# Kernel tuning notes

Measured on AMD Instinct MI355X. Metric: run time of the kernel, lower is better.

The kernel has to match this reference:

```python
import jax, jax.numpy as jnp
import numpy as np

E, H, V, KV, B, L = 512, 1024, 50257, 1000, 64, 512


def setup_inputs() -> dict:
    key = jax.random.key(0)
    ks = jax.random.split(key, 32)

    def p(i, shape, scale=0.02):
        return jax.random.normal(ks[i], shape, jnp.float32) * scale

    return {
        # forward args
        "input_ids": jax.random.randint(ks[0], (B,), 0, V),
        "h": p(1, (B, H), 1.0),
        "c": p(2, (B, H), 1.0),
        "k": p(3, (KV, E), 1.0),
        "context_vector": p(4, (B, H), 1.0),
        "encoder_outputs": p(5, (B, L, H), 1.0),
        # parameters (stored [in, out])
        "embedding": p(6, (V, E)),
        "W_ih": p(7, (E, 4 * H)),
        "W_hh": p(8, (H, 4 * H)),
        "b_ih": jnp.zeros((4 * H,), jnp.float32),
        "b_hh": jnp.zeros((4 * H,), jnp.float32),
        # attn MLP: Linear(2H,E) Tanh Linear(E,E) Tanh Linear(E,1)
        "aW1": p(9, (2 * H, E)), "ab1": jnp.zeros((E,), jnp.float32),
        "aW2": p(10, (E, E)), "ab2": jnp.zeros((E,), jnp.float32),
        "aW3": p(11, (E, 1)), "ab3": jnp.zeros((1,), jnp.float32),
        # attn_key MLP: Linear(E+2H,E) Tanh Linear(E,E) Tanh Linear(E,1)
        "kW1": p(12, (E + 2 * H, E)), "kb1": jnp.zeros((E,), jnp.float32),
        "kW2": p(13, (E, E)), "kb2": jnp.zeros((E,), jnp.float32),
        "kW3": p(14, (E, 1)), "kb3": jnp.zeros((1,), jnp.float32),
        # attn_linear: Linear(2H, V)
        "alW": p(15, (2 * H, V)), "alb": jnp.zeros((V,), jnp.float32),
    }


def reference(input_ids, h, c, k, context_vector, encoder_outputs,
              embedding, W_ih, W_hh, b_ih, b_hh,
              aW1, ab1, aW2, ab2, aW3, ab3,
              kW1, kb1, kW2, kb2, kW3, kb3,
              alW, alb):
    b = h.shape[0]
    kv = k.shape[0]
    v = alb.shape[0]

    # embedding lookup (dropout is identity in eval)
    x = embedding[input_ids]                                    # [B,E]

    # LSTMCell (PyTorch gate order: i, f, g, o)
    gates = x @ W_ih + h @ W_hh + b_ih + b_hh                   # [B,4H]
    i_g, f_g, g_g, o_g = jnp.split(gates, 4, axis=1)
    c_t = jax.nn.sigmoid(f_g) * c + jax.nn.sigmoid(i_g) * jnp.tanh(g_g)
    h_t = jax.nn.sigmoid(o_g) * jnp.tanh(c_t)                   # [B,H]

    # additive attention over encoder outputs
    h_ext = jnp.broadcast_to(h_t[:, None, :], encoder_outputs.shape)
    u = jnp.concatenate([encoder_outputs, h_ext], axis=2)       # [B,L,2H]
    u = jnp.tanh(u @ aW1 + ab1)
    u = jnp.tanh(u @ aW2 + ab2)
    u = (u @ aW3 + ab3)[..., 0]                                  # [B,L]
    a_t = jax.nn.softmax(u, axis=1)
    h_ctx = jnp.einsum('bl,blh->bh', a_t, encoder_outputs)       # [B,H]

    # key attention: cat(context, h_t, k) -> MLP -> [B,KV]
    ctx_ext = jnp.broadcast_to(context_vector[:, None, :], (b, kv, context_vector.shape[1]))
    ht_ext = jnp.broadcast_to(h_t[:, None, :], (b, kv, h_t.shape[1]))
    k_ext = jnp.broadcast_to(k[None, :, :], (b, kv, k.shape[1]))
    uk = jnp.concatenate([ctx_ext, ht_ext, k_ext], axis=2)       # [B,KV,E+2H]
    uk = jnp.tanh(uk @ kW1 + kb1)
    uk = jnp.tanh(uk @ kW2 + kb2)
    uk = (uk @ kW3 + kb3)[..., 0]                                # [B,KV]

    # zero-pad key logits into the full vocab (first V-KV entries are zero)
    v_k_t = jnp.concatenate([jnp.zeros((b, v - kv), h_t.dtype), uk], axis=1)

    # key_flag == 'True' path
    o_t = jnp.concatenate([h_t, h_ctx], axis=1) @ alW + alb + v_k_t  # [B,V]
    y_t = jax.nn.log_softmax(o_t, axis=1)
    return (y_t, h_t, c_t)
```

## Files before the change

### kernel.cpp

```cpp
#include <hip/hip_runtime.h>
#include <hip/hip_bf16.h>
#include <math.h>

#define EE 512
#define HH 1024
#define VV 50257
#define KVN 1000
#define BB 64
#define LL 512
#define FH 4096
#define TWOH 2048

typedef __hip_bfloat16 bf16;
typedef short bf16x8 __attribute__((ext_vector_type(8)));
typedef float f32x4  __attribute__((ext_vector_type(4)));

__device__ __forceinline__ float sigm(float x){ return 1.0f/(1.0f+__expf(-x)); }

__device__ __forceinline__ unsigned short f2bf(float f){
  unsigned int u = __float_as_uint(f);
  unsigned int r = (u + 0x7FFFu + ((u >> 16) & 1u)) >> 16;
  return (unsigned short)r;
}

__global__ __launch_bounds__(256)
void k_embed_gates(const int* __restrict__ ids, const float* __restrict__ h,
                   const float* __restrict__ emb,
                   const float* __restrict__ W_ih, const float* __restrict__ W_hh,
                   const float* __restrict__ b_ih, const float* __restrict__ b_hh,
                   float* __restrict__ gates){
  __shared__ float xh[8][1536];
  const int j  = blockIdx.x*256 + threadIdx.x;
  const int b0 = blockIdx.y*8;
  for (int t = threadIdx.x; t < 8*1536; t += 256){
    int bb = t / 1536, kk = t - bb*1536;
    int b = b0 + bb;
    float v;
    if (kk < EE) v = emb[(size_t)ids[b]*EE + kk];
    else         v = h[(size_t)b*HH + (kk-EE)];
    xh[bb][kk] = v;
  }
  __syncthreads();
  float acc[8];
  #pragma unroll
  for (int i=0;i<8;i++) acc[i]=0.f;
  for (int k=0;k<1536;k++){
    float w = (k<EE) ? W_ih[(size_t)k*FH + j] : W_hh[(size_t)(k-EE)*FH + j];
    #pragma unroll
    for (int i=0;i<8;i++) acc[i] += xh[i][k]*w;
  }
  const float bias = b_ih[j] + b_hh[j];
  #pragma unroll
  for (int i=0;i<8;i++) gates[(size_t)(b0+i)*FH + j] = acc[i] + bias;
}

__global__ __launch_bounds__(256)
void k_lstm(const float* __restrict__ gates, const float* __restrict__ c_in,
            float* __restrict__ hout, float* __restrict__ cout){
  int idx = blockIdx.x*256 + threadIdx.x;
  int b = idx >> 10, hh = idx & 1023;
  const float* g = gates + (size_t)b*FH;
  float ig = g[hh], fg = g[HH+hh], gg = g[2*HH+hh], og = g[3*HH+hh];
  float ct = sigm(fg)*c_in[idx] + sigm(ig)*tanhf(gg);
  float ht = sigm(og)*tanhf(ct);
  hout[idx] = ht;
  cout[idx] = ct;
}

__global__ __launch_bounds__(256)
void k_q1p1(const float* __restrict__ ht, const float* __restrict__ ctx,
            const float* __restrict__ aW1, const float* __restrict__ ab1,
            const float* __restrict__ kW1, const float* __restrict__ kb1,
            float* __restrict__ q1, float* __restrict__ p1){
  int e = blockIdx.x*256 + threadIdx.x;
  int b = blockIdx.y;
  float aq = 0.f, ap = 0.f;
  for (int k2 = 0; k2 < HH; ++k2){
    float hv = ht[(size_t)b*HH + k2];
    float cv = ctx[(size_t)b*HH + k2];
    aq += hv * aW1[(size_t)(HH+k2)*EE + e];
    ap += cv * kW1[(size_t)k2*EE + e];
    ap += hv * kW1[(size_t)(HH+k2)*EE + e];
  }
  q1[(size_t)b*EE + e] = aq + ab1[e];
  p1[(size_t)b*EE + e] = ap + kb1[e];
}

__global__ __launch_bounds__(256)
void k_p2(const float* __restrict__ kin, const float* __restrict__ kW1,
          float* __restrict__ p2){
  int e  = blockIdx.x*256 + threadIdx.x;
  int kv = blockIdx.y;
  float a = 0.f;
  for (int k2 = 0; k2 < EE; ++k2)
    a += kin[(size_t)kv*EE + k2] * kW1[(size_t)(TWOH+k2)*EE + e];
  p2[(size_t)kv*EE + e] = a;
}

__global__ __launch_bounds__(256)
void k_uk1(const float* __restrict__ p1, const float* __restrict__ p2,
           bf16* __restrict__ uk1){
  int idx = blockIdx.x*256 + threadIdx.x;
  int e   = idx & (EE-1);
  int r   = idx >> 9;
  int b   = r / KVN;
  int kv  = r - b*KVN;
  float v = tanhf(p1[(size_t)b*EE + e] + p2[(size_t)kv*EE + e]);
  uk1[idx] = __float2bfloat16(v);
}

__global__ __launch_bounds__(256)
void k_transpose_bf16(const float* __restrict__ W, bf16* __restrict__ Wt,
                      int K, int N){
  __shared__ float t[32][33];
  int k0 = blockIdx.y*32, n0 = blockIdx.x*32;
  int tx = threadIdx.x & 31, ty = threadIdx.x >> 5;
  #pragma unroll
  for (int i=0;i<4;i++){
    int kk = ty + i*8;
    t[kk][tx] = W[(size_t)(k0+kk)*N + n0 + tx];
  }
  __syncthreads();
  #pragma unroll
  for (int i=0;i<4;i++){
    int nn = ty + i*8;
    Wt[(size_t)(n0+nn)*K + k0 + tx] = __float2bfloat16(t[tx][nn]);
  }
}

__global__ __launch_bounds__(256)
void k_mfma_tanh_dot(const bf16* __restrict__ A, const bf16* __restrict__ Wt,
                     const float* __restrict__ bias, const float* __restrict__ w3,
                     float* __restrict__ logits){
  __shared__ short As[128*40];
  __shared__ short Bs[128*40];
  __shared__ float red[128*33];
  const int tid  = threadIdx.x;
  const int lane = tid & 63, wid = tid >> 6;
  const int wm = wid >> 1, wn = wid & 1;
  const int quad = lane >> 4, l16 = lane & 15;
  const int m0 = blockIdx.y*128, n0 = blockIdx.x*128;

  f32x4 acc[4][4] = {};
  for (int k0 = 0; k0 < 512; k0 += 32){
    #pragma unroll
    for (int it = 0; it < 2; ++it){
      int task = tid + it*256;
      int row = task >> 2, cg = task & 3;
      *(bf16x8*)(As + row*40 + cg*8) =
        *(const bf16x8*)((const short*)A + (size_t)(m0+row)*512 + k0 + cg*8);
      *(bf16x8*)(Bs + row*40 + cg*8) =
        *(const bf16x8*)((const short*)Wt + (size_t)(n0+row)*512 + k0 + cg*8);
    }
    __syncthreads();
    bf16x8 af[4], bfr[4];
    #pragma unroll
    for (int mt=0; mt<4; ++mt)
      af[mt] = *(const bf16x8*)(As + (wm*64 + mt*16 + l16)*40 + quad*8);
    #pragma unroll
    for (int nt=0; nt<4; ++nt)
      bfr[nt] = *(const bf16x8*)(Bs + (wn*64 + nt*16 + l16)*40 + quad*8);
    #pragma unroll
    for (int mt=0; mt<4; ++mt)
      #pragma unroll
      for (int nt=0; nt<4; ++nt)
        acc[mt][nt] = __builtin_amdgcn_mfma_f32_16x16x32_bf16(af[mt], bfr[nt], acc[mt][nt], 0, 0, 0);
    __syncthreads();
  }
  float bv[4], wv[4];
  #pragma unroll
  for (int nt=0; nt<4; ++nt){
    int n = n0 + wn*64 + nt*16 + l16;
    bv[nt] = bias[n]; wv[nt] = w3[n];
  }
  #pragma unroll
  for (int mt=0; mt<4; ++mt){
    #pragma unroll
    for (int r=0; r<4; ++r){
      float s = 0.f;
      #pragma unroll
      for (int nt=0; nt<4; ++nt)
        s += tanhf(acc[mt][nt][r] + bv[nt]) * wv[nt];
      int rowL = wm*64 + mt*16 + quad*4 + r;
      red[rowL*33 + wn*16 + l16] = s;
    }
  }
  __syncthreads();
  if (tid < 128){
    float s = 0.f;
    #pragma unroll
    for (int j=0;j<32;j++) s += red[tid*33 + j];
    atomicAdd(&logits[m0 + tid], s);
  }
}

__global__ __launch_bounds__(256)
void k_mfma_a1(const float* __restrict__ enc, const bf16* __restrict__ Wt,
               const float* __restrict__ q1, bf16* __restrict__ U1){
  __shared__ short As[128*40];
  __shared__ short Bs[128*40];
  const int tid  = threadIdx.x;
  const int lane = tid & 63, wid = tid >> 6;
  const int wm = wid >> 1, wn = wid & 1;
  const int quad = lane >> 4, l16 = lane & 15;
  const int m0 = blockIdx.y*128, n0 = blockIdx.x*128;

  f32x4 acc[4][4] = {};
  for (int k0 = 0; k0 < 1024; k0 += 32){
    #pragma unroll
    for (int it = 0; it < 4; ++it){
      int task = tid + it*256;
      int row = task >> 3, g = task & 7;
      float4 f = *(const float4*)(enc + (size_t)(m0+row)*1024 + k0 + g*4);
      uint2 pk;
      pk.x = (unsigned int)f2bf(f.x) | ((unsigned int)f2bf(f.y) << 16);
      pk.y = (unsigned int)f2bf(f.z) | ((unsigned int)f2bf(f.w) << 16);
      *(uint2*)(As + row*40 + g*4) = pk;
    }
    #pragma unroll
    for (int it = 0; it < 2; ++it){
      int task = tid + it*256;
      int row = task >> 2, cg = task & 3;
      *(bf16x8*)(Bs + row*40 + cg*8) =
        *(const bf16x8*)((const short*)Wt + (size_t)(n0+row)*1024 + k0 + cg*8);
    }
    __syncthreads();
    bf16x8 af[4], bfr[4];
    #pragma unroll
    for (int mt=0; mt<4; ++mt)
      af[mt] = *(const bf16x8*)(As + (wm*64 + mt*16 + l16)*40 + quad*8);
    #pragma unroll
    for (int nt=0; nt<4; ++nt)
      bfr[nt] = *(const bf16x8*)(Bs + (wn*64 + nt*16 + l16)*40 + quad*8);
    #pragma unroll
    for (int mt=0; mt<4; ++mt)
      #pragma unroll
      for (int nt=0; nt<4; ++nt)
        acc[mt][nt] = __builtin_amdgcn_mfma_f32_16x16x32_bf16(af[mt], bfr[nt], acc[mt][nt], 0, 0, 0);
    __syncthreads();
  }
  const int b = m0 >> 9;
  const float* q1r = q1 + (size_t)b*EE;
  #pragma unroll
  for (int mt=0; mt<4; ++mt){
    #pragma unroll
    for (int r=0; r<4; ++r){
      int m = m0 + wm*64 + mt*16 + quad*4 + r;
      #pragma unroll
      for (int nt=0; nt<4; ++nt){
        int n = n0 + wn*64 + nt*16 + l16;
        U1[(size_t)m*EE + n] = __float2bfloat16(tanhf(acc[mt][nt][r] + q1r[n]));
      }
    }
  }
}

__global__ __launch_bounds__(256)
void k_init_logits(float* __restrict__ ulog, float* __restrict__ uklog,
                   const float* __restrict__ ab3, const float* __restrict__ kb3){
  int i = blockIdx.x*256 + threadIdx.x;
  if (i < BB*LL)  ulog[i]  = ab3[0];
  if (i < BB*KVN) uklog[i] = kb3[0];
}

__global__ __launch_bounds__(256)
void k_softmax(float* __restrict__ ulog){
  __shared__ float sdata[256];
  int b = blockIdx.x, tid = threadIdx.x;
  float* row = ulog + (size_t)b*LL;
  float v0 = row[tid], v1 = row[tid+256];
  sdata[tid] = fmaxf(v0, v1);
  __syncthreads();
  for (int s=128;s>0;s>>=1){ if (tid<s) sdata[tid]=fmaxf(sdata[tid],sdata[tid+s]); __syncthreads(); }
  float mx = sdata[0];
  __syncthreads();
  float e0 = __expf(v0-mx), e1 = __expf(v1-mx);
  sdata[tid] = e0+e1;
  __syncthreads();
  for (int s=128;s>0;s>>=1){ if (tid<s) sdata[tid]+=sdata[tid+s]; __syncthreads(); }
  float inv = 1.f/sdata[0];
  row[tid]     = e0*inv;
  row[tid+256] = e1*inv;
}

__global__ __launch_bounds__(256)
void k_hctx(const float* __restrict__ a, const float* __restrict__ enc,
            float* __restrict__ hctx){
  int hh = blockIdx.x*256 + threadIdx.x;
  int b  = blockIdx.y;
  float s = 0.f;
  for (int l=0;l<LL;l++)
    s += a[(size_t)b*LL + l] * enc[((size_t)b*LL + l)*HH + hh];
  hctx[(size_t)b*HH + hh] = s;
}

__global__ __launch_bounds__(256)
void k_hcatT(const float* __restrict__ ht, const float* __restrict__ hctx,
             float* __restrict__ hcatT){
  int idx = blockIdx.x*256 + threadIdx.x;
  int b = idx & 63, kk = idx >> 6;
  float v = (kk < HH) ? ht[(size_t)b*HH + kk] : hctx[(size_t)b*HH + (kk-HH)];
  hcatT[idx] = v;
}

__global__ __launch_bounds__(256)
void k_final(const float* __restrict__ hcatT, const float* __restrict__ alW,
             const float* __restrict__ alb, const float* __restrict__ uklog,
             float* __restrict__ y){
  __shared__ float Hs[16][64];
  __shared__ float Ws[16][64];
  const int tid = threadIdx.x;
  const int tx = tid & 15, ty = tid >> 4;
  const int n0 = blockIdx.x * 64;
  float acc[4][4] = {};
  for (int k0 = 0; k0 < TWOH; k0 += 16){
    #pragma unroll
    for (int i=0;i<4;i++){
      int t = tid + i*256;
      int kk = t >> 6, cc = t & 63;
      Hs[kk][cc] = hcatT[(size_t)(k0+kk)*64 + cc];
      int v = n0 + cc;
      Ws[kk][cc] = (v < VV) ? alW[(size_t)(k0+kk)*VV + v] : 0.f;
    }
    __syncthreads();
    #pragma unroll
    for (int kk=0;kk<16;kk++){
      float4 hb = *(const float4*)(&Hs[kk][ty*4]);
      float4 wv = *(const float4*)(&Ws[kk][tx*4]);
      float ha[4] = {hb.x, hb.y, hb.z, hb.w};
      float wa[4] = {wv.x, wv.y, wv.z, wv.w};
      #pragma unroll
      for (int i=0;i<4;i++)
        #pragma unroll
        for (int j=0;j<4;j++)
          acc[i][j] += ha[i]*wa[j];
    }
    __syncthreads();
  }
  #pragma unroll
  for (int j=0;j<4;j++){
    int v = n0 + tx*4 + j;
    if (v < VV){
      float bias = alb[v];
      int dk = v - (VV - KVN);
      #pragma unroll
      for (int i=0;i<4;i++){
        int b = ty*4 + i;
        float o = acc[i][j] + bias;
        if (dk >= 0) o += uklog[b*KVN + dk];
        y[(size_t)b*VV + v] = o;
      }
    }
  }
}

__global__ __launch_bounds__(256)
void k_logsoftmax(float* __restrict__ y){
  __shared__ float sdata[256];
  int b = blockIdx.x, tid = threadIdx.x;
  float* row = y + (size_t)b*VV;
  float m = -1e30f;
  for (int i=tid;i<VV;i+=256) m = fmaxf(m, row[i]);
  sdata[tid] = m; __syncthreads();
  for (int s=128;s>0;s>>=1){ if (tid<s) sdata[tid]=fmaxf(sdata[tid],sdata[tid+s]); __syncthreads(); }
  float mx = sdata[0]; __syncthreads();
  float sum = 0.f;
  for (int i=tid;i<VV;i+=256) sum += __expf(row[i]-mx);
  sdata[tid] = sum; __syncthreads();
  for (int s=128;s>0;s>>=1){ if (tid<s) sdata[tid]+=sdata[tid+s]; __syncthreads(); }
  float lse = mx + logf(sdata[0]);
  for (int i=tid;i<VV;i+=256) row[i] -= lse;
}

extern "C" void kernel_launch(void* const* d_in, const int* in_sizes, int n_in,
                              void* d_out, int out_size, void* d_ws, size_t ws_size,
                              hipStream_t stream) {
  const int*   ids  = (const int*)  d_in[0];
  const float* h    = (const float*)d_in[1];
  const float* c    = (const float*)d_in[2];
  const float* kin  = (const float*)d_in[3];
  const float* ctx  = (const float*)d_in[4];
  const float* enc  = (const float*)d_in[5];
  const float* emb  = (const float*)d_in[6];
  const float* W_ih = (const float*)d_in[7];
  const float* W_hh = (const float*)d_in[8];
  const float* b_ih = (const float*)d_in[9];
  const float* b_hh = (const float*)d_in[10];
  const float* aW1  = (const float*)d_in[11];
  const float* ab1  = (const float*)d_in[12];
  const float* aW2  = (const float*)d_in[13];
  const float* ab2  = (const float*)d_in[14];
  const float* aW3  = (const float*)d_in[15];
  const float* ab3  = (const float*)d_in[16];
  const float* kW1  = (const float*)d_in[17];
  const float* kb1  = (const float*)d_in[18];
  const float* kW2  = (const float*)d_in[19];
  const float* kb2  = (const float*)d_in[20];
  const float* kW3  = (const float*)d_in[21];
  const float* kb3  = (const float*)d_in[22];
  const float* alW  = (const float*)d_in[23];
  const float* alb  = (const float*)d_in[24];

  float* y      = (float*)d_out;
  float* ht_out = y + (size_t)BB*VV;
  float* ct_out = ht_out + (size_t)BB*HH;

  char* w = (char*)d_ws;
  float* gates = (float*)w;  w += (size_t)BB*FH*4;
  float* q1    = (float*)w;  w += (size_t)BB*EE*4;
  float* p1    = (float*)w;  w += (size_t)BB*EE*4;
  float* p2    = (float*)w;  w += (size_t)KVN*EE*4;
  float* ulog  = (float*)w;  w += (size_t)BB*LL*4;
  float* uklog = (float*)w;  w += (size_t)BB*KVN*4;
  float* hctx  = (float*)w;  w += (size_t)BB*HH*4;
  float* hcatT = (float*)w;  w += (size_t)TWOH*BB*4;
  bf16*  U1    = (bf16*)w;   w += (size_t)BB*LL*EE*2;
  bf16*  UK1   = (bf16*)w;   w += (size_t)BB*KVN*EE*2;
  bf16*  aW1t  = (bf16*)w;   w += (size_t)EE*HH*2;
  bf16*  aW2t  = (bf16*)w;   w += (size_t)EE*EE*2;
  bf16*  kW2t  = (bf16*)w;   w += (size_t)EE*EE*2;

  k_transpose_bf16<<<dim3(EE/32, HH/32), 256, 0, stream>>>(aW1, aW1t, HH, EE);
  k_transpose_bf16<<<dim3(EE/32, EE/32), 256, 0, stream>>>(aW2, aW2t, EE, EE);
  k_transpose_bf16<<<dim3(EE/32, EE/32), 256, 0, stream>>>(kW2, kW2t, EE, EE);

  k_embed_gates<<<dim3(FH/256, BB/8), 256, 0, stream>>>(ids, h, emb, W_ih, W_hh, b_ih, b_hh, gates);
  k_lstm<<<(BB*HH)/256, 256, 0, stream>>>(gates, c, ht_out, ct_out);

  k_init_logits<<<(BB*KVN)/256 + 1, 256, 0, stream>>>(ulog, uklog, ab3, kb3);

  k_q1p1<<<dim3(EE/256, BB), 256, 0, stream>>>(ht_out, ctx, aW1, ab1, kW1, kb1, q1, p1);
  k_p2<<<dim3(EE/256, KVN), 256, 0, stream>>>(kin, kW1, p2);

  k_uk1<<<(BB*KVN*EE)/256, 256, 0, stream>>>(p1, p2, UK1);
  k_mfma_tanh_dot<<<dim3(4, (BB*KVN)/128), 256, 0, stream>>>(UK1, kW2t, kb2, kW3, uklog);

  k_mfma_a1<<<dim3(4, (BB*LL)/128), 256, 0, stream>>>(enc, aW1t, q1, U1);
  k_mfma_tanh_dot<<<dim3(4, (BB*LL)/128), 256, 0, stream>>>(U1, aW2t, ab2, aW3, ulog);
  k_softmax<<<BB, 256, 0, stream>>>(ulog);
  k_hctx<<<dim3(HH/256, BB), 256, 0, stream>>>(ulog, enc, hctx);

  k_hcatT<<<(TWOH*BB)/256, 256, 0, stream>>>(ht_out, hctx, hcatT);
  k_final<<<(VV + 63)/64, 256, 0, stream>>>(hcatT, alW, alb, uklog, y);
  k_logsoftmax<<<BB, 256, 0, stream>>>(y);
}
```

Baseline: 1.731 ms.

## Use MFMA for vocab projection, fuse key tanh, split-K gates, parallel log-softmax

Several independent changes at once. The final vocab projection now runs on bf16 MFMA with split-K and atomic accumulation into a bias-initialized output. The key-attention tanh is fused into the MFMA A-tile load, which removes the large UK1 intermediate. The LSTM gate GEMM is restructured into split-K tiles with atomics, and log-softmax is split into multi-block partial, combine and apply passes. The trade-offs are extra atomic traffic on the 64x50257 output, reduced precision on the vocab projection, and a tanh recomputed for every N-tile block.

```diff
diff --git a/kernel.cpp b/kernel.cpp
--- a/kernel.cpp
+++ b/kernel.cpp
@@ -24,34 +24,67 @@
 }
 
 __global__ __launch_bounds__(256)
+void k_gates_init(const float* __restrict__ b_ih, const float* __restrict__ b_hh,
+                  float* __restrict__ gates){
+  int i = blockIdx.x*256 + threadIdx.x;
+  int j = i & (FH-1);
+  gates[i] = b_ih[j] + b_hh[j];
+}
+
+__global__ __launch_bounds__(256)
 void k_embed_gates(const int* __restrict__ ids, const float* __restrict__ h,
                    const float* __restrict__ emb,
                    const float* __restrict__ W_ih, const float* __restrict__ W_hh,
-                   const float* __restrict__ b_ih, const float* __restrict__ b_hh,
                    float* __restrict__ gates){
-  __shared__ float xh[8][1536];
-  const int j  = blockIdx.x*256 + threadIdx.x;
-  const int b0 = blockIdx.y*8;
-  for (int t = threadIdx.x; t < 8*1536; t += 256){
-    int bb = t / 1536, kk = t - bb*1536;
-    int b = b0 + bb;
-    float v;
-    if (kk < EE) v = emb[(size_t)ids[b]*EE + kk];
-    else         v = h[(size_t)b*HH + (kk-EE)];
-    xh[bb][kk] = v;
+  __shared__ float Xs[64][68];
+  __shared__ float Ws[64][68];
+  const int tid = threadIdx.x;
+  const int nbase = blockIdx.x*64;
+  const int kbase = blockIdx.y*64;
+  {
+    int b = tid >> 2;
+    int kof = (tid & 3)*16;
+    int id = ids[b];
+    #pragma unroll
+    for (int i=0;i<16;i++){
+      int kg = kbase + kof + i;
+      float v = (kg < EE) ? emb[(size_t)id*EE + kg] : h[(size_t)b*HH + (kg-EE)];
+      Xs[kof+i][b] = v;
+    }
+  }
+  {
+    int n = tid & 63;
+    int kr0 = tid >> 6;
+    #pragma unroll
+    for (int i=0;i<16;i++){
+      int kr = kr0 + i*4;
+      int kg = kbase + kr;
+      float v = (kg < EE) ? W_ih[(size_t)kg*FH + nbase + n]
+                          : W_hh[(size_t)(kg-EE)*FH + nbase + n];
+      Ws[kr][n] = v;
+    }
   }
   __syncthreads();
-  float acc[8];
-  #pragma unroll
-  for (int i=0;i<8;i++) acc[i]=0.f;
-  for (int k=0;k<1536;k++){
-    float w = (k<EE) ? W_ih[(size_t)k*FH + j] : W_hh[(size_t)(k-EE)*FH + j];
-    #pragma unroll
-    for (int i=0;i<8;i++) acc[i] += xh[i][k]*w;
-  }
-  const float bias = b_ih[j] + b_hh[j];
-  #pragma unroll
-  for (int i=0;i<8;i++) gates[(size_t)(b0+i)*FH + j] = acc[i] + bias;
+  const int tx = tid & 15, ty = tid >> 4;
+  float acc[4][4] = {};
+  for (int k=0;k<64;k++){
+    float4 a4 = *(const float4*)(&Xs[k][ty*4]);
+    float4 w4 = *(const float4*)(&Ws[k][tx*4]);
+    float aa[4] = {a4.x,a4.y,a4.z,a4.w};
+    float ww[4] = {w4.x,w4.y,w4.z,w4.w};
+    #pragma unroll
+    for (int i=0;i<4;i++)
+      #pragma unroll
+      for (int j=0;j<4;j++)
+        acc[i][j] += aa[i]*ww[j];
+  }
+  #pragma unroll
+  for (int i=0;i<4;i++){
+    int b = ty*4 + i;
+    #pragma unroll
+    for (int j=0;j<4;j++)
+      atomicAdd(&gates[(size_t)b*FH + nbase + tx*4 + j], acc[i][j]);
+  }
 }
 
 __global__ __launch_bounds__(256)
@@ -98,18 +131,6 @@
 }
 
 __global__ __launch_bounds__(256)
-void k_uk1(const float* __restrict__ p1, const float* __restrict__ p2,
-           bf16* __restrict__ uk1){
-  int idx = blockIdx.x*256 + threadIdx.x;
-  int e   = idx & (EE-1);
-  int r   = idx >> 9;
-  int b   = r / KVN;
-  int kv  = r - b*KVN;
-  float v = tanhf(p1[(size_t)b*EE + e] + p2[(size_t)kv*EE + e]);
-  uk1[idx] = __float2bfloat16(v);
-}
-
-__global__ __launch_bounds__(256)
 void k_transpose_bf16(const float* __restrict__ W, bf16* __restrict__ Wt,
                       int K, int N){
   __shared__ float t[32][33];
@@ -134,7 +155,6 @@
                      float* __restrict__ logits){
   __shared__ short As[128*40];
   __shared__ short Bs[128*40];
-  __shared__ float red[128*33];
   const int tid  = threadIdx.x;
   const int lane = tid & 63, wid = tid >> 6;
   const int wm = wid >> 1, wn = wid & 1;
@@ -181,16 +201,88 @@
       #pragma unroll
       for (int nt=0; nt<4; ++nt)
         s += tanhf(acc[mt][nt][r] + bv[nt]) * wv[nt];
-      int rowL = wm*64 + mt*16 + quad*4 + r;
-      red[rowL*33 + wn*16 + l16] = s;
-    }
-  }
-  __syncthreads();
-  if (tid < 128){
-    float s = 0.f;
-    #pragma unroll
-    for (int j=0;j<32;j++) s += red[tid*33 + j];
-    atomicAdd(&logits[m0 + tid], s);
+      #pragma unroll
+      for (int off=8; off>=1; off>>=1) s += __shfl_xor(s, off, 16);
+      if (l16 == 0){
+        int row = wm*64 + mt*16 + quad*4 + r;
+        atomicAdd(&logits[m0 + row], s);
+      }
+    }
+  }
+}
+
+__global__ __launch_bounds__(256)
+void k_mfma_key(const float* __restrict__ p1, const float* __restrict__ p2,
+                const bf16* __restrict__ Wt,
+                const float* __restrict__ bias, const float* __restrict__ w3,
+                float* __restrict__ logits){
+  __shared__ short As[128*40];
+  __shared__ short Bs[128*40];
+  const int tid  = threadIdx.x;
+  const int lane = tid & 63, wid = tid >> 6;
+  const int wm = wid >> 1, wn = wid & 1;
+  const int quad = lane >> 4, l16 = lane & 15;
+  const int m0 = blockIdx.y*128, n0 = blockIdx.x*128;
+
+  f32x4 acc[4][4] = {};
+  for (int k0 = 0; k0 < 512; k0 += 32){
+    #pragma unroll
+    for (int it = 0; it < 2; ++it){
+      int grp = tid + it*256;
+      int row = grp >> 2, cg = grp & 3;
+      int r = m0 + row;
+      int b = r / KVN;
+      int kv = r - b*KVN;
+      int e = k0 + cg*8;
+      float4 a0 = *(const float4*)(p1 + (size_t)b*EE + e);
+      float4 a1 = *(const float4*)(p1 + (size_t)b*EE + e + 4);
+      float4 c0 = *(const float4*)(p2 + (size_t)kv*EE + e);
+      float4 c1 = *(const float4*)(p2 + (size_t)kv*EE + e + 4);
+      bf16x8 v;
+      v[0]=(short)f2bf(tanhf(a0.x+c0.x)); v[1]=(short)f2bf(tanhf(a0.y+c0.y));
+      v[2]=(short)f2bf(tanhf(a0.z+c0.z)); v[3]=(short)f2bf(tanhf(a0.w+c0.w));
+      v[4]=(short)f2bf(tanhf(a1.x+c1.x)); v[5]=(short)f2bf(tanhf(a1.y+c1.y));
+      v[6]=(short)f2bf(tanhf(a1.z+c1.z)); v[7]=(short)f2bf(tanhf(a1.w+c1.w));
+      *(bf16x8*)(As + row*40 + cg*8) = v;
+      *(bf16x8*)(Bs + row*40 + cg*8) =
+        *(const bf16x8*)((const short*)Wt + (size_t)(n0+row)*512 + k0 + cg*8);
+    }
+    __syncthreads();
+    bf16x8 af[4], bfr[4];
+    #pragma unroll
+    for (int mt=0; mt<4; ++mt)
+      af[mt] = *(const bf16x8*)(As + (wm*64 + mt*16 + l16)*40 + quad*8);
+    #pragma unroll
+    for (int nt=0; nt<4; ++nt)
+      bfr[nt] = *(const bf16x8*)(Bs + (wn*64 + nt*16 + l16)*40 + quad*8);
+    #pragma unroll
+    for (int mt=0; mt<4; ++mt)
+      #pragma unroll
+      for (int nt=0; nt<4; ++nt)
+        acc[mt][nt] = __builtin_amdgcn_mfma_f32_16x16x32_bf16(af[mt], bfr[nt], acc[mt][nt], 0, 0, 0);
+    __syncthreads();
+  }
+  float bv[4], wv[4];
+  #pragma unroll
+  for (int nt=0; nt<4; ++nt){
+    int n = n0 + wn*64 + nt*16 + l16;
+    bv[nt] = bias[n]; wv[nt] = w3[n];
+  }
+  #pragma unroll
+  for (int mt=0; mt<4; ++mt){
+    #pragma unroll
+    for (int r=0; r<4; ++r){
+      float s = 0.f;
+      #pragma unroll
+      for (int nt=0; nt<4; ++nt)
+        s += tanhf(acc[mt][nt][r] + bv[nt]) * wv[nt];
+      #pragma unroll
+      for (int off=8; off>=1; off>>=1) s += __shfl_xor(s, off, 16);
+      if (l16 == 0){
+        int row = wm*64 + mt*16 + quad*4 + r;
+        atomicAdd(&logits[m0 + row], s);
+      }
+    }
   }
 }
 
@@ -295,81 +387,138 @@
 }
 
 __global__ __launch_bounds__(256)
-void k_hcatT(const float* __restrict__ ht, const float* __restrict__ hctx,
-             float* __restrict__ hcatT){
+void k_hcat_bf16(const float* __restrict__ ht, const float* __restrict__ hctx,
+                 bf16* __restrict__ hcatb){
   int idx = blockIdx.x*256 + threadIdx.x;
-  int b = idx & 63, kk = idx >> 6;
+  int b = idx >> 11, kk = idx & 2047;
   float v = (kk < HH) ? ht[(size_t)b*HH + kk] : hctx[(size_t)b*HH + (kk-HH)];
-  hcatT[idx] = v;
-}
-
-__global__ __launch_bounds__(256)
-void k_final(const float* __restrict__ hcatT, const float* __restrict__ alW,
-             const float* __restrict__ alb, const float* __restrict__ uklog,
-             float* __restrict__ y){
-  __shared__ float Hs[16][64];
-  __shared__ float Ws[16][64];
-  const int tid = threadIdx.x;
-  const int tx = tid & 15, ty = tid >> 4;
-  const int n0 = blockIdx.x * 64;
-  float acc[4][4] = {};
-  for (int k0 = 0; k0 < TWOH; k0 += 16){
-    #pragma unroll
-    for (int i=0;i<4;i++){
-      int t = tid + i*256;
-      int kk = t >> 6, cc = t & 63;
-      Hs[kk][cc] = hcatT[(size_t)(k0+kk)*64 + cc];
-      int v = n0 + cc;
-      Ws[kk][cc] = (v < VV) ? alW[(size_t)(k0+kk)*VV + v] : 0.f;
-    }
-    __syncthreads();
-    #pragma unroll
-    for (int kk=0;kk<16;kk++){
-      float4 hb = *(const float4*)(&Hs[kk][ty*4]);
-      float4 wv = *(const float4*)(&Ws[kk][tx*4]);
-      float ha[4] = {hb.x, hb.y, hb.z, hb.w};
-      float wa[4] = {wv.x, wv.y, wv.z, wv.w};
-      #pragma unroll
-      for (int i=0;i<4;i++)
+  hcatb[idx] = __float2bfloat16(v);
+}
+
+__global__ __launch_bounds__(256)
+void k_y_init(const float* __restrict__ alb, const float* __restrict__ uklog,
+              float* __restrict__ y){
+  int idx = blockIdx.x*256 + threadIdx.x;
+  if (idx >= BB*VV) return;
+  int b = idx / VV;
+  int v = idx - b*VV;
+  float o = alb[v];
+  int dk = v - (VV - KVN);
+  if (dk >= 0) o += uklog[b*KVN + dk];
+  y[idx] = o;
+}
+
+__global__ __launch_bounds__(256)
+void k_final_mfma(const bf16* __restrict__ hcatb, const float* __restrict__ alW,
+                  float* __restrict__ y){
+  __shared__ short As[64*40];
+  __shared__ float Bs[32*133];
+  const int tid  = threadIdx.x;
+  const int lane = tid & 63, wid = tid >> 6;
+  const int quad = lane >> 4, l16 = lane & 15;
+  const int n0 = blockIdx.x*128;
+  const int kc0 = blockIdx.y*512;
+
+  f32x4 acc[4][2] = {};
+  for (int k0 = 0; k0 < 512; k0 += 32){
+    {
+      int row = tid >> 2, cg = tid & 3;
+      *(bf16x8*)(As + row*40 + cg*8) =
+        *(const bf16x8*)((const short*)hcatb + (size_t)row*TWOH + kc0 + k0 + cg*8);
+    }
+    #pragma unroll
+    for (int i=0;i<16;i++){
+      int flat = tid + i*256;
+      int kk = flat >> 7, n = flat & 127;
+      int gv = n0 + n;
+      float v = (gv < VV) ? alW[(size_t)(kc0 + k0 + kk)*VV + gv] : 0.f;
+      Bs[kk*133 + n] = v;
+    }
+    __syncthreads();
+    bf16x8 af[4], bfr[2];
+    #pragma unroll
+    for (int mt=0; mt<4; ++mt)
+      af[mt] = *(const bf16x8*)(As + (mt*16 + l16)*40 + quad*8);
+    #pragma unroll
+    for (int nt=0; nt<2; ++nt){
+      int nloc = wid*32 + nt*16 + l16;
+      bf16x8 v;
+      #pragma unroll
+      for (int j=0;j<8;j++)
+        v[j] = (short)f2bf(Bs[(quad*8 + j)*133 + nloc]);
+      bfr[nt] = v;
+    }
+    #pragma unroll
+    for (int mt=0; mt<4; ++mt)
+      #pragma unroll
+      for (int nt=0; nt<2; ++nt)
+        acc[mt][nt] = __builtin_amdgcn_mfma_f32_16x16x32_bf16(af[mt], bfr[nt], acc[mt][nt], 0, 0, 0);
+    __syncthreads();
+  }
+  #pragma unroll
+  for (int nt=0; nt<2; ++nt){
+    int v = n0 + wid*32 + nt*16 + l16;
+    if (v < VV){
+      #pragma unroll
+      for (int mt=0; mt<4; ++mt){
         #pragma unroll
-        for (int j=0;j<4;j++)
-          acc[i][j] += ha[i]*wa[j];
-    }
-    __syncthreads();
-  }
-  #pragma unroll
-  for (int j=0;j<4;j++){
-    int v = n0 + tx*4 + j;
-    if (v < VV){
-      float bias = alb[v];
-      int dk = v - (VV - KVN);
-      #pragma unroll
-      for (int i=0;i<4;i++){
-        int b = ty*4 + i;
-        float o = acc[i][j] + bias;
-        if (dk >= 0) o += uklog[b*KVN + dk];
-        y[(size_t)b*VV + v] = o;
+        for (int r=0; r<4; ++r){
+          int b = mt*16 + quad*4 + r;
+          atomicAdd(&y[(size_t)b*VV + v], acc[mt][nt][r]);
+        }
       }
     }
   }
 }
 
-__global__ __launch_bounds__(256)
-void k_logsoftmax(float* __restrict__ y){
-  __shared__ float sdata[256];
-  int b = blockIdx.x, tid = threadIdx.x;
-  float* row = y + (size_t)b*VV;
+#define LSE_CH 6283
+__global__ __launch_bounds__(256)
+void k_lse_part(const float* __restrict__ y, float* __restrict__ pmax,
+                float* __restrict__ psum){
+  __shared__ float sm[256], ss[256];
+  int b = blockIdx.y, chunk = blockIdx.x, tid = threadIdx.x;
+  int start = chunk*LSE_CH;
+  int end = start + LSE_CH; if (end > VV) end = VV;
+  const float* row = y + (size_t)b*VV;
+  float m = -1e30f, s = 0.f;
+  for (int i = start + tid; i < end; i += 256){
+    float v = row[i];
+    if (v > m){ s = s*__expf(m - v) + 1.f; m = v; }
+    else s += __expf(v - m);
+  }
+  sm[tid] = m; ss[tid] = s;
+  __syncthreads();
+  for (int st=128; st>0; st>>=1){
+    if (tid < st){
+      float m2 = sm[tid+st], s2 = ss[tid+st];
+      float M = fmaxf(sm[tid], m2);
+      ss[tid] = ss[tid]*__expf(sm[tid]-M) + s2*__expf(m2-M);
+      sm[tid] = M;
+    }
+    __syncthreads();
+  }
+  if (tid == 0){ pmax[b*8 + chunk] = sm[0]; psum[b*8 + chunk] = ss[0]; }
+}
+
+__global__ __launch_bounds__(64)
+void k_lse_combine(const float* __restrict__ pmax, const float* __restrict__ psum,
+                   float* __restrict__ lse){
+  int b = threadIdx.x;
   float m = -1e30f;
-  for (int i=tid;i<VV;i+=256) m = fmaxf(m, row[i]);
-  sdata[tid] = m; __syncthreads();
-  for (int s=128;s>0;s>>=1){ if (tid<s) sdata[tid]=fmaxf(sdata[tid],sdata[tid+s]); __syncthreads(); }
-  float mx = sdata[0]; __syncthreads();
-  float sum = 0.f;
-  for (int i=tid;i<VV;i+=256) sum += __expf(row[i]-mx);
-  sdata[tid] = sum; __syncthreads();
-  for (int s=128;s>0;s>>=1){ if (tid<s) sdata[tid]+=sdata[tid+s]; __syncthreads(); }
-  float lse = mx + logf(sdata[0]);
-  for (int i=tid;i<VV;i+=256) row[i] -= lse;
+  #pragma unroll
+  for (int i=0;i<8;i++) m = fmaxf(m, pmax[b*8+i]);
+  float s = 0.f;
+  #pragma unroll
+  for (int i=0;i<8;i++) s += psum[b*8+i]*__expf(pmax[b*8+i]-m);
+  lse[b] = m + logf(s);
+}
+
+__global__ __launch_bounds__(256)
+void k_lse_apply(float* __restrict__ y, const float* __restrict__ lse){
+  int idx = blockIdx.x*256 + threadIdx.x;
+  if (idx >= BB*VV) return;
+  int b = idx / VV;
+  y[idx] -= lse[b];
 }
 
 extern "C" void kernel_launch(void* const* d_in, const int* in_sizes, int n_in,
@@ -413,18 +562,23 @@
   float* ulog  = (float*)w;  w += (size_t)BB*LL*4;
   float* uklog = (float*)w;  w += (size_t)BB*KVN*4;
   float* hctx  = (float*)w;  w += (size_t)BB*HH*4;
-  float* hcatT = (float*)w;  w += (size_t)TWOH*BB*4;
+  bf16*  hcatb = (bf16*)w;   w += (size_t)BB*TWOH*2;
   bf16*  U1    = (bf16*)w;   w += (size_t)BB*LL*EE*2;
-  bf16*  UK1   = (bf16*)w;   w += (size_t)BB*KVN*EE*2;
   bf16*  aW1t  = (bf16*)w;   w += (size_t)EE*HH*2;
   bf16*  aW2t  = (bf16*)w;   w += (size_t)EE*EE*2;
   bf16*  kW2t  = (bf16*)w;   w += (size_t)EE*EE*2;
+  float* pmax  = (float*)w;  w += (size_t)BB*8*4;
+  float* psum  = (float*)w;  w += (size_t)BB*8*4;
+  float* lse   = (float*)w;  w += (size_t)BB*4;
+
+  const int NBLK = (BB*VV + 255)/256;
 
   k_transpose_bf16<<<dim3(EE/32, HH/32), 256, 0, stream>>>(aW1, aW1t, HH, EE);
   k_transpose_bf16<<<dim3(EE/32, EE/32), 256, 0, stream>>>(aW2, aW2t, EE, EE);
   k_transpose_bf16<<<dim3(EE/32, EE/32), 256, 0, stream>>>(kW2, kW2t, EE, EE);
 
-  k_embed_gates<<<dim3(FH/256, BB/8), 256, 0, stream>>>(ids, h, emb, W_ih, W_hh, b_ih, b_hh, gates);
+  k_gates_init<<<(BB*FH)/256, 256, 0, stream>>>(b_ih, b_hh, gates);
+  k_embed_gates<<<dim3(FH/64, (EE+HH)/64), 256, 0, stream>>>(ids, h, emb, W_ih, W_hh, gates);
   k_lstm<<<(BB*HH)/256, 256, 0, stream>>>(gates, c, ht_out, ct_out);
 
   k_init_logits<<<(BB*KVN)/256 + 1, 256, 0, stream>>>(ulog, uklog, ab3, kb3);
@@ -432,15 +586,17 @@
   k_q1p1<<<dim3(EE/256, BB), 256, 0, stream>>>(ht_out, ctx, aW1, ab1, kW1, kb1, q1, p1);
   k_p2<<<dim3(EE/256, KVN), 256, 0, stream>>>(kin, kW1, p2);
 
-  k_uk1<<<(BB*KVN*EE)/256, 256, 0, stream>>>(p1, p2, UK1);
-  k_mfma_tanh_dot<<<dim3(4, (BB*KVN)/128), 256, 0, stream>>>(UK1, kW2t, kb2, kW3, uklog);
+  k_mfma_key<<<dim3(4, (BB*KVN)/128), 256, 0, stream>>>(p1, p2, kW2t, kb2, kW3, uklog);
 
   k_mfma_a1<<<dim3(4, (BB*LL)/128), 256, 0, stream>>>(enc, aW1t, q1, U1);
   k_mfma_tanh_dot<<<dim3(4, (BB*LL)/128), 256, 0, stream>>>(U1, aW2t, ab2, aW3, ulog);
   k_softmax<<<BB, 256, 0, stream>>>(ulog);
   k_hctx<<<dim3(HH/256, BB), 256, 0, stream>>>(ulog, enc, hctx);
 
-  k_hcatT<<<(TWOH*BB)/256, 256, 0, stream>>>(ht_out, hctx, hcatT);
-  k_final<<<(VV + 63)/64, 256, 0, stream>>>(hcatT, alW, alb, uklog, y);
-  k_logsoftmax<<<BB, 256, 0, stream>>>(y);
-}
+  k_hcat_bf16<<<(BB*TWOH)/256, 256, 0, stream>>>(ht_out, hctx, hcatb);
+  k_y_init<<<NBLK, 256, 0, stream>>>(alb, uklog, y);
+  k_final_mfma<<<dim3((VV+127)/128, 4), 256, 0, stream>>>(hcatb, alW, y);
+  k_lse_part<<<dim3(8, BB), 256, 0, stream>>>(y, pmax, psum);
+  k_lse_combine<<<1, 64, 0, stream>>>(pmax, psum, lse);
+  k_lse_apply<<<NBLK, 256, 0, stream>>>(y, lse);
+}
```

After: 1.458 ms. 1.19x faster.
